# Performance work log

Measured on AMD Instinct MI355X. Metric: run time of the kernel, lower is better.

The kernel has to match this reference:

```python
import jax, jax.numpy as jnp
from jax import lax
import numpy as np

BATCH, T, N, S = 512, 1024, 64, 32


def setup_inputs() -> dict:
    key = jax.random.key(0)
    k1, k2, k3, k4 = jax.random.split(key, 4)
    return {
        "inputs": jax.random.uniform(k1, (BATCH, T, S), dtype=jnp.float32),
        "emission_kernel": jax.random.normal(k2, (N, S), dtype=jnp.float32),
        "transition_kernel": jax.random.normal(k3, (N, N), dtype=jnp.float32),
        "init_kernel": jax.random.normal(k4, (N,), dtype=jnp.float32),
    }


def reference(inputs, emission_kernel, transition_kernel, init_kernel):
    # HMM forward algorithm with per-step normalization (scaled forward vars).
    A = jax.nn.softmax(transition_kernel, axis=-1)   # [n, n] transition
    B = jax.nn.softmax(emission_kernel, axis=-1)     # [n, s] emission
    I = jax.nn.softmax(init_kernel, axis=-1)         # [n]   initial dist

    batch, n = inputs.shape[0], A.shape[0]
    # Emission likelihoods for all timesteps at once (same math as per-step matvec)
    E_all = jnp.einsum('ns,bts->tbn', B, inputs)     # [T, batch, n]

    def step(carry, e_t):
        is_init, fwd, loglik = carry
        # R = is_init * I  +  A^T @ fwd   (matvec(A, fwd, transpose_a=True))
        R = is_init[:, None] * I[None, :] + fwd @ A          # [batch, n]
        f = e_t * R                                          # [batch, n]
        Ssum = jnp.sum(f, axis=-1)                           # [batch]
        loglik = loglik + jnp.log(Ssum)
        f = f / Ssum[:, None]
        return (jnp.zeros_like(is_init), f, loglik), (f, loglik)

    init = (jnp.ones((batch,), dtype=jnp.float32),
            jnp.zeros((batch, n), dtype=jnp.float32),
            jnp.zeros((batch,), dtype=jnp.float32))
    _, (fwds, lls) = lax.scan(step, init, E_all)
    fwds = jnp.swapaxes(fwds, 0, 1)                  # [batch, T, n]
    lls = jnp.swapaxes(lls, 0, 1)                    # [batch, T]
    # Pack (forward vars, running loglik) into one array: [batch, T, n+1]
    return jnp.concatenate([fwds, lls[..., None]], axis=-1)
```

## Files before the change

### kernel.cpp

```cpp
#include <hip/hip_runtime.h>

#define BATCH 512
#define TT    1024
#define NST   64
#define NSYM  32
#define NCH   64
#define CLEN  16
#define WARM  16
#define LN2F  0.69314718055994530942f

#define AP_MV    6400
#define AP_EM    8448
#define WS_STATS 9472

typedef _Float16 f16x8 __attribute__((ext_vector_type(8)));
typedef float    f32x4 __attribute__((ext_vector_type(4)));

#define MFMA_F16(a,b,c) __builtin_amdgcn_mfma_f32_16x16x32_f16(a,b,c,0,0,0)

__device__ __forceinline__ unsigned pkrtz_u(float a, float b) {
    return __builtin_bit_cast(unsigned, __builtin_amdgcn_cvt_pkrtz(a, b));
}

__device__ __forceinline__ int sigma_k(int g, int r) {
    return (r < 4) ? (4 * g + r) : (16 + 4 * g + (r - 4));
}

__device__ __forceinline__ f16x8 pk8(float a0, float a1, float a2, float a3,
                                     float a4, float a5, float a6, float a7) {
    union U { unsigned u[4]; f16x8 v; } u;
    u.u[0] = pkrtz_u(a0, a1);
    u.u[1] = pkrtz_u(a2, a3);
    u.u[2] = pkrtz_u(a4, a5);
    u.u[3] = pkrtz_u(a6, a7);
    return u.v;
}

__global__ __launch_bounds__(64) void hmm_prep(
    const float* __restrict__ em, const float* __restrict__ tr,
    const float* __restrict__ ini, float* __restrict__ ws)
{
    const int n = threadIdx.x;

    {
        float a[64];
        float m = -1e30f;
        #pragma unroll
        for (int j = 0; j < 64; ++j) { a[j] = tr[n * 64 + j]; m = fmaxf(m, a[j]); }
        float s = 0.f;
        #pragma unroll
        for (int j = 0; j < 64; ++j) { a[j] = __expf(a[j] - m); s += a[j]; }
        const float inv = 1.f / s;
        #pragma unroll
        for (int j = 0; j < 64; ++j) ws[n * 64 + j] = a[j] * inv;
    }
    {
        float bv[32];
        float m = -1e30f;
        #pragma unroll
        for (int j = 0; j < 32; ++j) { bv[j] = em[n * 32 + j]; m = fmaxf(m, bv[j]); }
        float s = 0.f;
        #pragma unroll
        for (int j = 0; j < 32; ++j) { bv[j] = __expf(bv[j] - m); s += bv[j]; }
        const float inv = 1.f / s;
        #pragma unroll
        for (int j = 0; j < 32; ++j) ws[4096 + n * 32 + j] = bv[j] * inv;
    }
    {
        float v = ini[n];
        float m = v;
        #pragma unroll
        for (int off = 32; off; off >>= 1) m = fmaxf(m, __shfl_xor(m, off, 64));
        const float e = __expf(v - m);
        float s = e;
        #pragma unroll
        for (int off = 32; off; off >>= 1) s += __shfl_xor(s, off, 64);
        ws[6144 + n] = e / s;
    }

    __syncthreads();

    const int g   = n >> 4;
    const int cl  = n & 15;
    unsigned* wsu = (unsigned*)ws;

    #pragma unroll
    for (int mt = 0; mt < 4; ++mt) {
        #pragma unroll
        for (int kc = 0; kc < 2; ++kc) {
            #pragma unroll
            for (int p = 0; p < 4; ++p) {
                const int k0 = sigma_k(g, 2 * p);
                const int k1 = sigma_k(g, 2 * p + 1);
                const int m  = 16 * mt + cl;
                const float a0 = ws[(32 * kc + k0) * 64 + m];
                const float a1 = ws[(32 * kc + k1) * 64 + m];
                wsu[AP_MV + ((mt * 2 + kc) * 64 + n) * 4 + p] = pkrtz_u(a0, a1);
            }
        }
        #pragma unroll
        for (int p = 0; p < 4; ++p) {
            const int k0 = sigma_k(g, 2 * p);
            const int k1 = sigma_k(g, 2 * p + 1);
            const int st = 16 * mt + cl;
            const float b0 = ws[4096 + st * 32 + k0];
            const float b1 = ws[4096 + st * 32 + k1];
            wsu[AP_EM + (mt * 64 + n) * 4 + p] = pkrtz_u(b0, b1);
        }
    }
}

__global__ __launch_bounds__(64, 1) void hmm_scan(
    const float* __restrict__ inputs, float* __restrict__ ws,
    float* __restrict__ out)
{
    const int lane = threadIdx.x;
    const int col  = lane & 15;
    const int g    = lane >> 4;
    const int b    = blockIdx.x >> 2;
    const int w    = blockIdx.x & 3;
    const int c    = 16 * w + col;
    const int t0   = c * CLEN;
    const bool isc0 = (c == 0);

    f16x8 Amv[4][2], Aem[4];
    {
        const int4* mvp = (const int4*)((const unsigned*)ws + AP_MV);
        #pragma unroll
        for (int mt = 0; mt < 4; ++mt)
            #pragma unroll
            for (int kc = 0; kc < 2; ++kc)
                Amv[mt][kc] = __builtin_bit_cast(f16x8, mvp[(mt * 2 + kc) * 64 + lane]);
        const int4* emp = (const int4*)((const unsigned*)ws + AP_EM);
        #pragma unroll
        for (int mt = 0; mt < 4; ++mt)
            Aem[mt] = __builtin_bit_cast(f16x8, emp[mt * 64 + lane]);
    }

    const float* __restrict__ xp = inputs + (size_t)b * (TT * NSYM);
    float* __restrict__ op       = out    + (size_t)b * (TT * 65);

    float4 rga[4], rgb[4];
    auto loadx = [&](int k, int s) {
        int t = t0 + k;
        t = t < 0 ? 0 : t;
        t = t > TT - 1 ? TT - 1 : t;
        const float* row = xp + (size_t)t * NSYM;
        rga[s] = *(const float4*)(row + 4 * g);
        rgb[s] = *(const float4*)(row + 16 + 4 * g);
    };

    float hD[4][4];
    #pragma unroll
    for (int mt = 0; mt < 4; ++mt)
        #pragma unroll
        for (int r = 0; r < 4; ++r) hD[mt][r] = 1.0f;
    int Esum = 0;

    const f32x4 z4 = {0.f, 0.f, 0.f, 0.f};

    auto step = [&](int k, int s, bool store_) {
        if (store_) {
            float p = 0.f;
            #pragma unroll
            for (int mt = 0; mt < 4; ++mt)
                #pragma unroll
                for (int r = 0; r < 4; ++r) p += hD[mt][r];
            p += __shfl_xor(p, 16, 64);
            p += __shfl_xor(p, 32, 64);
            const float rS = __builtin_amdgcn_rcpf(p);
            float* rowp = op + (size_t)(t0 + k - 1) * 65;
            #pragma unroll
            for (int mt = 0; mt < 4; ++mt) {
                const float4 v4 = {hD[mt][0] * rS, hD[mt][1] * rS,
                                   hD[mt][2] * rS, hD[mt][3] * rS};
                *(float4*)(rowp + 16 * mt + 4 * g) = v4;
            }
            if (g == 0) rowp[64] = __logf(p) + (float)Esum * LN2F;
        }
        const int pb = __builtin_amdgcn_readlane(__float_as_int(hD[0][0]), 15);
        int ex = (pb >> 23) & 255;
        ex = ex < 1 ? 1 : (ex > 253 ? 253 : ex);
        const float sc = __uint_as_float((unsigned)(254 - ex) << 23);
        Esum += ex - 127;
        const f16x8 bx = pk8(rga[s].x, rga[s].y, rga[s].z, rga[s].w,
                             rgb[s].x, rgb[s].y, rgb[s].z, rgb[s].w);
        f32x4 E[4];
        #pragma unroll
        for (int mt = 0; mt < 4; ++mt) E[mt] = MFMA_F16(Aem[mt], bx, z4);
        const f16x8 bh0 = pk8(hD[0][0], hD[0][1], hD[0][2], hD[0][3],
                              hD[1][0], hD[1][1], hD[1][2], hD[1][3]);
        const f16x8 bh1 = pk8(hD[2][0], hD[2][1], hD[2][2], hD[2][3],
                              hD[3][0], hD[3][1], hD[3][2], hD[3][3]);
        f32x4 mv[4];
        #pragma unroll
        for (int mt = 0; mt < 4; ++mt) {
            mv[mt] = MFMA_F16(Amv[mt][0], bh0, z4);
            mv[mt] = MFMA_F16(Amv[mt][1], bh1, mv[mt]);
        }
        #pragma unroll
        for (int mt = 0; mt < 4; ++mt)
            #pragma unroll
            for (int r = 0; r < 4; ++r)
                hD[mt][r] = (E[mt][r] * sc) * mv[mt][r];
        loadx(k + 4, s);
    };

    #pragma unroll
    for (int s = 0; s < 4; ++s) loadx(-WARM + s, s);

    for (int kk = -WARM; kk < 0; kk += 4) {
        #pragma unroll
        for (int s = 0; s < 4; ++s) step(kk + s, s, false);
    }

    float Lstart;
    {
        float p = 0.f;
        #pragma unroll
        for (int mt = 0; mt < 4; ++mt)
            #pragma unroll
            for (int r = 0; r < 4; ++r) p += hD[mt][r];
        p += __shfl_xor(p, 16, 64);
        p += __shfl_xor(p, 32, 64);
        Lstart = __logf(p) + (float)Esum * LN2F;
    }
    Lstart = isc0 ? 0.f : Lstart;

    step(0, 0, false);

    {
        const float* row = xp;
        const float4 xa = *(const float4*)(row + 4 * g);
        const float4 xb = *(const float4*)(row + 16 + 4 * g);
        const f16x8 bx0 = pk8(xa.x, xa.y, xa.z, xa.w, xb.x, xb.y, xb.z, xb.w);
        #pragma unroll
        for (int mt = 0; mt < 4; ++mt) {
            const f32x4 E0 = MFMA_F16(Aem[mt], bx0, z4);
            const float4 iv = *(const float4*)(ws + 6144 + 16 * mt + 4 * g);
            const float ivv[4] = {iv.x, iv.y, iv.z, iv.w};
            #pragma unroll
            for (int r = 0; r < 4; ++r)
                if (isc0) hD[mt][r] = E0[r] * ivv[r];
        }
        if (isc0) Esum = 0;
    }

    #pragma unroll
    for (int s = 1; s < 4; ++s) step(s, s, true);
    #pragma unroll
    for (int kk = 4; kk <= 12; kk += 4) {
        #pragma unroll
        for (int s = 0; s < 4; ++s) step(kk + s, s, true);
    }

    {
        float p = 0.f;
        #pragma unroll
        for (int mt = 0; mt < 4; ++mt)
            #pragma unroll
            for (int r = 0; r < 4; ++r) p += hD[mt][r];
        p += __shfl_xor(p, 16, 64);
        p += __shfl_xor(p, 32, 64);
        const float rS = __builtin_amdgcn_rcpf(p);
        float* rowp = op + (size_t)(t0 + CLEN - 1) * 65;
        #pragma unroll
        for (int mt = 0; mt < 4; ++mt) {
            const float4 v4 = {hD[mt][0] * rS, hD[mt][1] * rS,
                               hD[mt][2] * rS, hD[mt][3] * rS};
            *(float4*)(rowp + 16 * mt + 4 * g) = v4;
        }
        if (g == 0) {
            rowp[64] = __logf(p) + (float)Esum * LN2F;
            ws[WS_STATS + (size_t)b * NCH + c] = Lstart;
        }
    }
}

__global__ __launch_bounds__(64) void hmm_fix(
    const float* __restrict__ ws, float* __restrict__ out)
{
    const int b    = blockIdx.x;
    const int lane = threadIdx.x;

    float* __restrict__ op = out + (size_t)b * (TT * 65);

    const float Ls = ws[WS_STATS + (size_t)b * NCH + lane];
    const float Le = op[(size_t)(lane * CLEN + CLEN - 1) * 65 + 64];
    const float D  = Le - Ls;

    float O = 0.f;
    #pragma unroll
    for (int j = 0; j < NCH - 1; ++j) {
        const float Dj = __int_as_float(
            __builtin_amdgcn_readlane(__float_as_int(D), j));
        if (lane > j) O += Dj;
    }
    const float offs = O - Ls;

    #pragma unroll
    for (int k = 0; k < 16; ++k) {
        const int row  = k * 64 + lane;
        const int cidx = row >> 4;
        const float offk = __shfl(offs, cidx, 64);
        op[(size_t)row * 65 + 64] += offk;
    }
}

extern "C" void kernel_launch(void* const* d_in, const int* in_sizes, int n_in,
                              void* d_out, int out_size, void* d_ws, size_t ws_size,
                              hipStream_t stream) {
    const float* inputs = (const float*)d_in[0];
    const float* em     = (const float*)d_in[1];
    const float* tr     = (const float*)d_in[2];
    const float* ini    = (const float*)d_in[3];
    float* out = (float*)d_out;
    float* ws  = (float*)d_ws;

    hmm_prep<<<1, 64, 0, stream>>>(em, tr, ini, ws);
    hmm_scan<<<BATCH * 4, 64, 0, stream>>>(inputs, ws, out);
    hmm_fix<<<BATCH, 64, 0, stream>>>(ws, out);
}
```

Baseline: 68.33 us.

## Shorten warmup, stage weights through LDS, and split MFMA accumulation chains

Cuts the warm-up recurrence from 16 to 12 steps, which reduces redundant serial work per chunk but may weaken convergence of the chunked forward state. It loads the packed transition and emission fragments through shared memory with a barrier before moving them into registers. The matvec no longer chains two dependent MFMAs: each half is computed independently and the results are summed in VALU, which shortens the per-step critical path. The emission scale factor is also applied right after the emission MFMA rather than in the final product.

```diff
diff --git a/kernel.cpp b/kernel.cpp
--- a/kernel.cpp
+++ b/kernel.cpp
@@ -6,7 +6,7 @@
 #define NSYM  32
 #define NCH   64
 #define CLEN  16
-#define WARM  16
+#define WARM  12
 #define LN2F  0.69314718055994530942f
 
 #define AP_MV    6400
@@ -123,18 +123,25 @@
     const int t0   = c * CLEN;
     const bool isc0 = (c == 0);
 
+    __shared__ int4 fl[12][64];
     f16x8 Amv[4][2], Aem[4];
     {
         const int4* mvp = (const int4*)((const unsigned*)ws + AP_MV);
+        const int4* emp = (const int4*)((const unsigned*)ws + AP_EM);
+        #pragma unroll
+        for (int j = 0; j < 8; ++j) fl[j][lane] = mvp[j * 64 + lane];
+        #pragma unroll
+        for (int j = 0; j < 4; ++j) fl[8 + j][lane] = emp[j * 64 + lane];
+        __syncthreads();
+        #pragma unroll
+        for (int mt = 0; mt < 4; ++mt) {
+            Amv[mt][0] = __builtin_bit_cast(f16x8, fl[mt * 2 + 0][lane]);
+            Amv[mt][1] = __builtin_bit_cast(f16x8, fl[mt * 2 + 1][lane]);
+            Aem[mt]    = __builtin_bit_cast(f16x8, fl[8 + mt][lane]);
+        }
         #pragma unroll
         for (int mt = 0; mt < 4; ++mt)
-            #pragma unroll
-            for (int kc = 0; kc < 2; ++kc)
-                Amv[mt][kc] = __builtin_bit_cast(f16x8, mvp[(mt * 2 + kc) * 64 + lane]);
-        const int4* emp = (const int4*)((const unsigned*)ws + AP_EM);
-        #pragma unroll
-        for (int mt = 0; mt < 4; ++mt)
-            Aem[mt] = __builtin_bit_cast(f16x8, emp[mt * 64 + lane]);
+            asm volatile("" : "+v"(Amv[mt][0]), "+v"(Amv[mt][1]), "+v"(Aem[mt]));
     }
 
     const float* __restrict__ xp = inputs + (size_t)b * (TT * NSYM);
@@ -185,24 +192,28 @@
         Esum += ex - 127;
         const f16x8 bx = pk8(rga[s].x, rga[s].y, rga[s].z, rga[s].w,
                              rgb[s].x, rgb[s].y, rgb[s].z, rgb[s].w);
-        f32x4 E[4];
-        #pragma unroll
-        for (int mt = 0; mt < 4; ++mt) E[mt] = MFMA_F16(Aem[mt], bx, z4);
+        f32x4 Esc[4];
+        #pragma unroll
+        for (int mt = 0; mt < 4; ++mt) {
+            const f32x4 E = MFMA_F16(Aem[mt], bx, z4);
+            Esc[mt][0] = E[0] * sc; Esc[mt][1] = E[1] * sc;
+            Esc[mt][2] = E[2] * sc; Esc[mt][3] = E[3] * sc;
+        }
         const f16x8 bh0 = pk8(hD[0][0], hD[0][1], hD[0][2], hD[0][3],
                               hD[1][0], hD[1][1], hD[1][2], hD[1][3]);
         const f16x8 bh1 = pk8(hD[2][0], hD[2][1], hD[2][2], hD[2][3],
                               hD[3][0], hD[3][1], hD[3][2], hD[3][3]);
-        f32x4 mv[4];
-        #pragma unroll
-        for (int mt = 0; mt < 4; ++mt) {
-            mv[mt] = MFMA_F16(Amv[mt][0], bh0, z4);
-            mv[mt] = MFMA_F16(Amv[mt][1], bh1, mv[mt]);
+        f32x4 mva[4], mvb[4];
+        #pragma unroll
+        for (int mt = 0; mt < 4; ++mt) {
+            mva[mt] = MFMA_F16(Amv[mt][0], bh0, z4);
+            mvb[mt] = MFMA_F16(Amv[mt][1], bh1, z4);
         }
         #pragma unroll
         for (int mt = 0; mt < 4; ++mt)
             #pragma unroll
             for (int r = 0; r < 4; ++r)
-                hD[mt][r] = (E[mt][r] * sc) * mv[mt][r];
+                hD[mt][r] = Esc[mt][r] * (mva[mt][r] + mvb[mt][r]);
         loadx(k + 4, s);
     };
 
```

Measured after the change: 70.07 us. 1.03x slower.
